# Kernel tuning notes

Measured on AMD Instinct MI355X. Metric: run time of the kernel, lower is better.

The kernel has to match this reference:

```python
import jax, jax.numpy as jnp
import numpy as np

B, C, H, W = 16, 128, 128, 128
NUM_HEADS, HEAD_DIM = 4, 32
HIDDEN = NUM_HEADS * HEAD_DIM  # 128
GROUPS = 32
EPS = 1e-5


def setup_inputs() -> dict:
    key = jax.random.key(0)
    ks = jax.random.split(key, 6)
    # conv1x1 weights: torch Conv2d weight (out, in, 1, 1) -> stored as (out, in)
    fan_qkv = C
    fan_proj = HIDDEN
    return {
        "x": jax.random.normal(ks[0], (B, C, H, W), dtype=jnp.float32),
        "gn_w": jnp.ones((C,), dtype=jnp.float32),
        "gn_b": jnp.zeros((C,), dtype=jnp.float32),
        "qkv_w": jax.random.normal(ks[1], (3 * HIDDEN, C), dtype=jnp.float32) / np.sqrt(fan_qkv),
        "proj_w": jax.random.normal(ks[2], (C, HIDDEN), dtype=jnp.float32) / np.sqrt(fan_proj),
        "proj_b": jax.random.normal(ks[3], (C,), dtype=jnp.float32) * 0.01,
    }


def reference(x, gn_w, gn_b, qkv_w, proj_w, proj_b):
    b, c, h, w = x.shape
    n = h * w
    residual = x
    # GroupNorm(32 groups), biased variance, affine
    xg = x.reshape(b, GROUPS, c // GROUPS, h, w)
    mu = xg.mean(axis=(2, 3, 4), keepdims=True)
    var = xg.var(axis=(2, 3, 4), keepdims=True)
    xn = ((xg - mu) * jax.lax.rsqrt(var + EPS)).reshape(b, c, h, w)
    xn = xn * gn_w[None, :, None, None] + gn_b[None, :, None, None]
    # 1x1 conv QKV (no bias); channel layout -> (b, 3, heads, head_dim, n)
    qkv = jnp.einsum('oc,bchw->bohw', qkv_w, xn)
    qkv = qkv.reshape(b, 3, NUM_HEADS, HEAD_DIM, n)
    q, k, v = qkv[:, 0], qkv[:, 1], qkv[:, 2]
    q = jax.nn.softmax(q, axis=-1)   # over spatial positions
    k = jax.nn.softmax(k, axis=-2)   # over head_dim
    # context = k @ v^T : (b,h,D,D)
    ctx = jnp.einsum('bhdn,bhen->bhde', k, v)
    # out = context^T @ q : (b,h,D,n)
    out = jnp.einsum('bhde,bhdn->bhen', ctx, q)
    out = out.reshape(b, HIDDEN, h, w)
    # 1x1 conv projection (with bias)
    out = jnp.einsum('co,bohw->bchw', proj_w, out) + proj_b[None, :, None, None]
    return out + residual
```

## Files before the change

### kernel.cpp

```cpp
#include <hip/hip_runtime.h>


#define B_ 16
#define C_ 128
#define N_ 16384

typedef short bf16x8 __attribute__((ext_vector_type(8)));
typedef float f32x4 __attribute__((ext_vector_type(4)));
typedef unsigned u32x2 __attribute__((ext_vector_type(2)));

__device__ __forceinline__ ushort f2bf(float f) {
    union { float f; unsigned u; } v; v.f = f;
    unsigned r = (v.u + 0x7FFFu + ((v.u >> 16) & 1u)) >> 16;
    return (ushort)r;
}
__device__ __forceinline__ float bf2f(unsigned h) {
    union { unsigned u; float f; } v; v.u = h << 16;
    return v.f;
}

__global__ void k_stats(const float* __restrict__ x, const float* __restrict__ gnw,
                        const float* __restrict__ gnb, float* __restrict__ sc,
                        float* __restrict__ bi,
                        const float* __restrict__ qkvw, ushort* __restrict__ wbf) {
    int bg = blockIdx.x;
    if (bg >= 512) {
        int i = (bg - 512) * 1024 + threadIdx.x;
        if (i < 384 * 128) wbf[i] = f2bf(qkvw[i]);
        return;
    }
    const float4* p = (const float4*)(x + (size_t)bg * (4 * N_));
    float s = 0.f, s2 = 0.f;
    for (int i = threadIdx.x; i < N_; i += 1024) {
        float4 v = p[i];
        s  += v.x + v.y + v.z + v.w;
        s2 += v.x * v.x + v.y * v.y + v.z * v.z + v.w * v.w;
    }
    #pragma unroll
    for (int d = 32; d > 0; d >>= 1) { s += __shfl_xor(s, d); s2 += __shfl_xor(s2, d); }
    __shared__ float ls[16], ls2[16];
    int wid = threadIdx.x >> 6, lane = threadIdx.x & 63;
    if (lane == 0) { ls[wid] = s; ls2[wid] = s2; }
    __syncthreads();
    if (threadIdx.x == 0) {
        float S = 0.f, S2 = 0.f;
        #pragma unroll
        for (int i = 0; i < 16; ++i) { S += ls[i]; S2 += ls2[i]; }
        float m = S / 65536.f;
        float var = S2 / 65536.f - m * m;
        float rs = rsqrtf(var + 1e-5f);
        int b = bg >> 5, g = bg & 31;
        #pragma unroll
        for (int i = 0; i < 4; ++i) {
            int c = g * 4 + i;
            float scv = rs * gnw[c];
            sc[b * 128 + c] = scv;
            bi[b * 128 + c] = gnb[c] - m * scv;
        }
    }
}


#define MFMA16(A, Bv, Cc) __builtin_amdgcn_mfma_f32_16x16x32_bf16(A, Bv, Cc, 0, 0, 0)

#define DO_Q(J, OT) do { \
    f32x4 acc = {0.f, 0.f, 0.f, 0.f}; \
    acc = MFMA16(wf[J][0], xb[0], acc); acc = MFMA16(wf[J][1], xb[1], acc); \
    acc = MFMA16(wf[J][2], xb[2], acc); acc = MFMA16(wf[J][3], xb[3], acc); \
    float e0 = __expf(acc[0]), e1 = __expf(acc[1]); \
    float e2 = __expf(acc[2]), e3 = __expf(acc[3]); \
    qacc[J][0] += e0; qacc[J][1] += e1; qacc[J][2] += e2; qacc[J][3] += e3; \
    u32x2 pkq; \
    pkq.x = (unsigned)f2bf(e0) | ((unsigned)f2bf(e1) << 16); \
    pkq.y = (unsigned)f2bf(e2) | ((unsigned)f2bf(e3) << 16); \
    *(u32x2*)(eqp + (OT) * 16) = pkq; \
} while (0)

#define DO_K(JLO, H) do { \
    f32x4 aL = {0.f, 0.f, 0.f, 0.f}, aH = {0.f, 0.f, 0.f, 0.f}; \
    aL = MFMA16(wf[JLO][0], xb[0], aL);     aH = MFMA16(wf[(JLO)+1][0], xb[0], aH); \
    aL = MFMA16(wf[JLO][1], xb[1], aL);     aH = MFMA16(wf[(JLO)+1][1], xb[1], aH); \
    aL = MFMA16(wf[JLO][2], xb[2], aL);     aH = MFMA16(wf[(JLO)+1][2], xb[2], aH); \
    aL = MFMA16(wf[JLO][3], xb[3], aL);     aH = MFMA16(wf[(JLO)+1][3], xb[3], aH); \
    float eL0 = __expf(aL[0]), eL1 = __expf(aL[1]), eL2 = __expf(aL[2]), eL3 = __expf(aL[3]); \
    float eH0 = __expf(aH[0]), eH1 = __expf(aH[1]), eH2 = __expf(aH[2]), eH3 = __expf(aH[3]); \
    float s = eL0 + eL1 + eL2 + eL3 + eH0 + eH1 + eH2 + eH3; \
    s += __shfl_xor(s, 16); s += __shfl_xor(s, 32); \
    float rinv = 1.f / s; \
    ksm[H][lg * 4 + 0][nloc] = f2bf(eL0 * rinv); \
    ksm[H][lg * 4 + 1][nloc] = f2bf(eL1 * rinv); \
    ksm[H][lg * 4 + 2][nloc] = f2bf(eL2 * rinv); \
    ksm[H][lg * 4 + 3][nloc] = f2bf(eL3 * rinv); \
    ksm[H][16 + lg * 4 + 0][nloc] = f2bf(eH0 * rinv); \
    ksm[H][16 + lg * 4 + 1][nloc] = f2bf(eH1 * rinv); \
    ksm[H][16 + lg * 4 + 2][nloc] = f2bf(eH2 * rinv); \
    ksm[H][16 + lg * 4 + 3][nloc] = f2bf(eH3 * rinv); \
} while (0)

#define DO_V(J, HV, EB) do { \
    f32x4 acc = {0.f, 0.f, 0.f, 0.f}; \
    acc = MFMA16(wf[J][0], xb[0], acc); acc = MFMA16(wf[J][1], xb[1], acc); \
    acc = MFMA16(wf[J][2], xb[2], acc); acc = MFMA16(wf[J][3], xb[3], acc); \
    vls[HV][(EB) + lg * 4 + 0][nloc] = f2bf(acc[0]); \
    vls[HV][(EB) + lg * 4 + 1][nloc] = f2bf(acc[1]); \
    vls[HV][(EB) + lg * 4 + 2][nloc] = f2bf(acc[2]); \
    vls[HV][(EB) + lg * 4 + 3][nloc] = f2bf(acc[3]); \
} while (0)

__global__ __launch_bounds__(256, 2) void k_main(
    const float* __restrict__ x, const ushort* __restrict__ wbf,
    const float* __restrict__ scA, const float* __restrict__ biA,
    ushort* __restrict__ eqT, float* __restrict__ qsumP, float* __restrict__ ctxP) {
    int blk = blockIdx.x;
    int b = blk >> 6, nb = blk & 63;
    int tid = threadIdx.x, wid = tid >> 6, lane = tid & 63;
    int l15 = lane & 15, lg = lane >> 4;

    __shared__ __align__(16) ushort xs[4096];
    __shared__ __align__(16) ushort ksm[4][32][40];
    __shared__ __align__(16) ushort vls[4][32][40];

    bf16x8 wf[6][4];
    {
        const ushort* wr = wbf + (size_t)(wid * 96 + l15) * 128 + lg * 8;
        #pragma unroll
        for (int j = 0; j < 6; ++j)
            #pragma unroll
            for (int kc = 0; kc < 4; ++kc)
                wf[j][kc] = *(const bf16x8*)(wr + j * 2048 + kc * 32);
    }

    float qacc[6][4];
    #pragma unroll
    for (int j = 0; j < 6; ++j)
        #pragma unroll
        for (int r = 0; r < 4; ++r) qacc[j][r] = 0.f;
    f32x4 cacc[2][2];
    #pragma unroll
    for (int di = 0; di < 2; ++di)
        #pragma unroll
        for (int ei = 0; ei < 2; ++ei) cacc[di][ei] = (f32x4){0.f, 0.f, 0.f, 0.f};

    const int pk_ = tid & 7, pcb = tid >> 3;
    const float* xrow = x + (size_t)b * (C_ * N_) + nb * 256 + pk_ * 4;
    float scv[4], biv[4];
    #pragma unroll
    for (int i = 0; i < 4; ++i) {
        scv[i] = scA[b * 128 + pcb * 4 + i];
        biv[i] = biA[b * 128 + pcb * 4 + i];
    }
    unsigned boffj[4];
    #pragma unroll
    for (int j = 0; j < 4; ++j) {
        int n = pk_ * 4 + j;
        boffj[j] = (unsigned)(n * 256 + (((pcb >> 1) * 16) ^ ((n & 7) << 4)) + (pcb & 1) * 8);
    }

    for (int ch = 0; ch < 8; ++ch) {
        __syncthreads();
        unsigned e[4][4];
        #pragma unroll
        for (int i = 0; i < 4; ++i) {
            float4 v = *(const float4*)(xrow + (size_t)(pcb * 4 + i) * N_ + ch * 32);
            float s = scv[i], t = biv[i];
            e[i][0] = f2bf(v.x * s + t);
            e[i][1] = f2bf(v.y * s + t);
            e[i][2] = f2bf(v.z * s + t);
            e[i][3] = f2bf(v.w * s + t);
        }
        #pragma unroll
        for (int j = 0; j < 4; ++j) {
            u32x2 wj;
            wj.x = e[0][j] | (e[1][j] << 16);
            wj.y = e[2][j] | (e[3][j] << 16);
            *(u32x2*)((char*)xs + boffj[j]) = wj;
        }
        __syncthreads();

        #pragma unroll
        for (int nt = 0; nt < 2; ++nt) {
            int row = nt * 16 + l15;
            bf16x8 xb[4];
            #pragma unroll
            for (int kc = 0; kc < 4; ++kc) {
                unsigned off = (unsigned)(row * 256 +
                    (((kc * 4 + lg) * 16) ^ ((row & 7) << 4)));
                xb[kc] = *(const bf16x8*)((const char*)xs + off);
            }
            int nloc = nt * 16 + l15;
            int ng = nb * 256 + ch * 32 + nloc;
            ushort* eqp = eqT + ((size_t)b * N_ + ng) * 128 + lg * 4;

            if (wid == 0) {
                DO_Q(0, 0); DO_Q(1, 1); DO_Q(2, 2); DO_Q(3, 3); DO_Q(4, 4); DO_Q(5, 5);
            } else if (wid == 1) {
                DO_Q(0, 6); DO_Q(1, 7); DO_K(2, 0); DO_K(4, 1);
            } else if (wid == 2) {
                DO_K(0, 2); DO_K(2, 3); DO_V(4, 0, 0); DO_V(5, 0, 16);
            } else {
                DO_V(0, 1, 0); DO_V(1, 1, 16); DO_V(2, 2, 0);
                DO_V(3, 2, 16); DO_V(4, 3, 0); DO_V(5, 3, 16);
            }
        }
        __syncthreads();

        {
            bf16x8 A0 = *(const bf16x8*)&ksm[wid][l15][lg * 8];
            bf16x8 A1 = *(const bf16x8*)&ksm[wid][16 + l15][lg * 8];
            bf16x8 B0 = *(const bf16x8*)&vls[wid][l15][lg * 8];
            bf16x8 B1 = *(const bf16x8*)&vls[wid][16 + l15][lg * 8];
            cacc[0][0] = MFMA16(A0, B0, cacc[0][0]);
            cacc[0][1] = MFMA16(A0, B1, cacc[0][1]);
            cacc[1][0] = MFMA16(A1, B0, cacc[1][0]);
            cacc[1][1] = MFMA16(A1, B1, cacc[1][1]);
        }
    }

    int nq = (wid == 0) ? 6 : (wid == 1 ? 2 : 0);
    #pragma unroll
    for (int j = 0; j < 6; ++j) {
        if (j < nq) {
            #pragma unroll
            for (int r = 0; r < 4; ++r) {
                float s = qacc[j][r];
                s += __shfl_xor(s, 1); s += __shfl_xor(s, 2);
                s += __shfl_xor(s, 4); s += __shfl_xor(s, 8);
                if (l15 == 0)
                    qsumP[(size_t)blk * 128 + (wid * 6 + j) * 16 + lg * 4 + r] = s;
            }
        }
    }
    float* cp = ctxP + (size_t)blk * 4096 + wid * 1024;
    #pragma unroll
    for (int di = 0; di < 2; ++di)
        #pragma unroll
        for (int ei = 0; ei < 2; ++ei)
            #pragma unroll
            for (int r = 0; r < 4; ++r)
                cp[(di * 16 + lg * 4 + r) * 32 + ei * 16 + l15] = cacc[di][ei][r];
}

__global__ void k_red(float* __restrict__ ctxP) {
    int blk = blockIdx.x;
    int b = blk >> 3, sl = blk & 7;
    float* base = ctxP + (size_t)b * 64 * 4096;
    #pragma unroll
    for (int r = 0; r < 2; ++r) {
        int i = sl * 512 + r * 256 + threadIdx.x;
        float s = 0.f;
        for (int q = 0; q < 64; ++q) s += base[(size_t)q * 4096 + i];
        base[i] = s;
    }
}

__global__ void k_comb(const float* __restrict__ ctxP, const float* __restrict__ qsumP,
                       const float* __restrict__ projw, ushort* __restrict__ mpp) {
    int b = blockIdx.x, tid = threadIdx.x;
    __shared__ float ctx[4096];
    __shared__ float qinv[128];
    for (int i = tid; i < 4096; i += 256)
        ctx[i] = ctxP[(size_t)b * 64 * 4096 + i];
    if (tid < 128) {
        float s = 0.f;
        const float* p = qsumP + (size_t)b * 64 * 128 + tid;
        for (int q = 0; q < 64; ++q) s += p[q * 128];
        qinv[tid] = 1.f / s;
    }
    __syncthreads();
    int c = tid >> 1, hd0 = (tid & 1) * 64;
    unsigned ow[32];
    for (int k = 0; k < 64; ++k) {
        int hd = hd0 + k, h = hd >> 5, d = hd & 31;
        const float* pw = projw + c * 128 + h * 32;
        const float* cx = ctx + h * 1024 + d * 32;
        float s = 0.f;
        #pragma unroll 8
        for (int e = 0; e < 32; ++e) s += pw[e] * cx[e];
        s *= qinv[hd];
        ushort bv = f2bf(s);
        if (k & 1) ow[k >> 1] |= ((unsigned)bv) << 16; else ow[k >> 1] = bv;
    }
    ushort* dst = mpp + ((size_t)(b * 128 + c)) * 128 + hd0;
    #pragma unroll
    for (int q = 0; q < 8; ++q) {
        uint4 t; t.x = ow[q * 4]; t.y = ow[q * 4 + 1]; t.z = ow[q * 4 + 2]; t.w = ow[q * 4 + 3];
        ((uint4*)dst)[q] = t;
    }
}

__global__ __launch_bounds__(256) void k_final(
    const ushort* __restrict__ eqT, const ushort* __restrict__ mpp,
    const float* __restrict__ projb, const float* __restrict__ x,
    float* __restrict__ out) {
    int blk = blockIdx.x;
    int b = blk >> 7, nb = blk & 127;
    int tid = threadIdx.x, wid = tid >> 6, lane = tid & 63;
    int l15 = lane & 15, lg = lane >> 4;

    __shared__ __align__(16) ushort att[16384];

    bf16x8 bm[2][4];
    #pragma unroll
    for (int ctk = 0; ctk < 2; ++ctk) {
        const ushort* br = mpp + ((size_t)(b * 128 + (wid * 2 + ctk) * 16 + l15)) * 128 + lg * 8;
        #pragma unroll
        for (int kc = 0; kc < 4; ++kc) bm[ctk][kc] = *(const bf16x8*)(br + kc * 32);
    }

    int n0 = nb * 128;
    #pragma unroll
    for (int nt = 0; nt < 8; ++nt) {
        const ushort* ar = eqT + ((size_t)b * N_ + n0 + nt * 16 + l15) * 128 + lg * 8;
        bf16x8 af[4];
        #pragma unroll
        for (int kc = 0; kc < 4; ++kc) af[kc] = *(const bf16x8*)(ar + kc * 32);
        #pragma unroll
        for (int ctk = 0; ctk < 2; ++ctk) {
            f32x4 a = {0.f, 0.f, 0.f, 0.f};
            #pragma unroll
            for (int kc = 0; kc < 4; ++kc) a = MFMA16(af[kc], bm[ctk][kc], a);
            int c = (wid * 2 + ctk) * 16 + l15;
            int nloc = nt * 16 + lg * 4;
            unsigned byte = (unsigned)(c * 256 + ((nloc * 2) ^ ((c & 15) << 4)));
            u32x2 pk;
            pk.x = (unsigned)f2bf(a[0]) | ((unsigned)f2bf(a[1]) << 16);
            pk.y = (unsigned)f2bf(a[2]) | ((unsigned)f2bf(a[3]) << 16);
            *(u32x2*)((char*)att + byte) = pk;
        }
    }
    __syncthreads();

    int crow = lane >> 5;
    int n4 = (lane & 31) * 4;
    #pragma unroll
    for (int it = 0; it < 16; ++it) {
        int c = wid * 32 + it * 2 + crow;
        unsigned byte = (unsigned)(c * 256 + ((n4 * 2) ^ ((c & 15) << 4)));
        u32x2 pk = *(const u32x2*)((const char*)att + byte);
        size_t off = (size_t)(b * C_ + c) * N_ + n0 + n4;
        f32x4 xv = __builtin_nontemporal_load((const f32x4*)(x + off));
        float pbv = projb[c];
        f32x4 o4;
        o4[0] = bf2f(pk.x & 0xffffu) + pbv + xv[0];
        o4[1] = bf2f(pk.x >> 16)     + pbv + xv[1];
        o4[2] = bf2f(pk.y & 0xffffu) + pbv + xv[2];
        o4[3] = bf2f(pk.y >> 16)     + pbv + xv[3];
        *(f32x4*)(out + off) = o4;
    }
}

extern "C" void kernel_launch(void* const* d_in, const int* in_sizes, int n_in,
                              void* d_out, int out_size, void* d_ws, size_t ws_size,
                              hipStream_t stream) {
    const float* x     = (const float*)d_in[0];
    const float* gnw   = (const float*)d_in[1];
    const float* gnb   = (const float*)d_in[2];
    const float* qkvw  = (const float*)d_in[3];
    const float* projw = (const float*)d_in[4];
    const float* projb = (const float*)d_in[5];
    float* out = (float*)d_out;

    char* ws = (char*)d_ws;
    ushort* wbf   = (ushort*)(ws);
    float*  qsumP = (float*)(ws + 102400);
    ushort* mpp   = (ushort*)(ws + 626688);
    float*  sc    = (float*)(ws + 626688);
    float*  bi    = (float*)(ws + 634880);
    float*  ctxP  = (float*)(ws + 1150976);
    ushort* eqT   = (ushort*)(ws + 17928192);

    k_stats<<<560,  1024, 0, stream>>>(x, gnw, gnb, sc, bi, qkvw, wbf);
    k_main <<<1024, 256,  0, stream>>>(x, wbf, sc, bi, eqT, qsumP, ctxP);
    k_red  <<<128,  256,  0, stream>>>(ctxP);
    k_comb <<<16,   256,  0, stream>>>(ctxP, qsumP, projw, mpp);
    k_final<<<2048, 256,  0, stream>>>(eqT, mpp, projb, x, out);
}
```

Measured before the change: 234.8 us.

## Recompute softmax-Q numerators in final kernel instead of storing eqT

k_main no longer writes the exp(q) tensor to global memory and only accumulates its column sums. k_final reloads x, applies the GroupNorm scale/bias, recomputes the Q projection and exponent into LDS, then applies the combined context/projection matrix. This removes a large bf16 intermediate's write and read traffic, at the cost of an extra x read and duplicated Q MFMA/exp work in k_final. The workspace is relaid out so scale/bias no longer alias the mpp buffer.

```diff
diff --git a/kernel.cpp b/kernel.cpp
--- a/kernel.cpp
+++ b/kernel.cpp
@@ -63,17 +63,12 @@
 
 #define MFMA16(A, Bv, Cc) __builtin_amdgcn_mfma_f32_16x16x32_bf16(A, Bv, Cc, 0, 0, 0)
 
-#define DO_Q(J, OT) do { \
+#define DO_Q(J) do { \
     f32x4 acc = {0.f, 0.f, 0.f, 0.f}; \
     acc = MFMA16(wf[J][0], xb[0], acc); acc = MFMA16(wf[J][1], xb[1], acc); \
     acc = MFMA16(wf[J][2], xb[2], acc); acc = MFMA16(wf[J][3], xb[3], acc); \
-    float e0 = __expf(acc[0]), e1 = __expf(acc[1]); \
-    float e2 = __expf(acc[2]), e3 = __expf(acc[3]); \
-    qacc[J][0] += e0; qacc[J][1] += e1; qacc[J][2] += e2; qacc[J][3] += e3; \
-    u32x2 pkq; \
-    pkq.x = (unsigned)f2bf(e0) | ((unsigned)f2bf(e1) << 16); \
-    pkq.y = (unsigned)f2bf(e2) | ((unsigned)f2bf(e3) << 16); \
-    *(u32x2*)(eqp + (OT) * 16) = pkq; \
+    qacc[J][0] += __expf(acc[0]); qacc[J][1] += __expf(acc[1]); \
+    qacc[J][2] += __expf(acc[2]); qacc[J][3] += __expf(acc[3]); \
 } while (0)
 
 #define DO_K(JLO, H) do { \
@@ -110,7 +105,7 @@
 __global__ __launch_bounds__(256, 2) void k_main(
     const float* __restrict__ x, const ushort* __restrict__ wbf,
     const float* __restrict__ scA, const float* __restrict__ biA,
-    ushort* __restrict__ eqT, float* __restrict__ qsumP, float* __restrict__ ctxP) {
+    float* __restrict__ qsumP, float* __restrict__ ctxP) {
     int blk = blockIdx.x;
     int b = blk >> 6, nb = blk & 63;
     int tid = threadIdx.x, wid = tid >> 6, lane = tid & 63;
@@ -188,13 +183,11 @@
                 xb[kc] = *(const bf16x8*)((const char*)xs + off);
             }
             int nloc = nt * 16 + l15;
-            int ng = nb * 256 + ch * 32 + nloc;
-            ushort* eqp = eqT + ((size_t)b * N_ + ng) * 128 + lg * 4;
 
             if (wid == 0) {
-                DO_Q(0, 0); DO_Q(1, 1); DO_Q(2, 2); DO_Q(3, 3); DO_Q(4, 4); DO_Q(5, 5);
+                DO_Q(0); DO_Q(1); DO_Q(2); DO_Q(3); DO_Q(4); DO_Q(5);
             } else if (wid == 1) {
-                DO_Q(0, 6); DO_Q(1, 7); DO_K(2, 0); DO_K(4, 1);
+                DO_Q(0); DO_Q(1); DO_K(2, 0); DO_K(4, 1);
             } else if (wid == 2) {
                 DO_K(0, 2); DO_K(2, 3); DO_V(4, 0, 0); DO_V(5, 0, 16);
             } else {
@@ -289,16 +282,28 @@
 }
 
 __global__ __launch_bounds__(256) void k_final(
-    const ushort* __restrict__ eqT, const ushort* __restrict__ mpp,
+    const ushort* __restrict__ wbf, const ushort* __restrict__ mpp,
+    const float* __restrict__ scA, const float* __restrict__ biA,
     const float* __restrict__ projb, const float* __restrict__ x,
     float* __restrict__ out) {
     int blk = blockIdx.x;
-    int b = blk >> 7, nb = blk & 127;
+    int b = blk >> 8, nb = blk & 255;
     int tid = threadIdx.x, wid = tid >> 6, lane = tid & 63;
     int l15 = lane & 15, lg = lane >> 4;
-
-    __shared__ __align__(16) ushort att[16384];
-
+    int n0 = nb * 64;
+
+    __shared__ __align__(16) char lds[32768];
+    ushort* xs   = (ushort*)lds;
+    ushort* att  = (ushort*)lds;
+    ushort* eqls = (ushort*)(lds + 16384);
+
+    bf16x8 wq[2][4];
+    #pragma unroll
+    for (int j = 0; j < 2; ++j) {
+        const ushort* wr = wbf + (size_t)((wid * 2 + j) * 16 + l15) * 128 + lg * 8;
+        #pragma unroll
+        for (int kc = 0; kc < 4; ++kc) wq[j][kc] = *(const bf16x8*)(wr + kc * 32);
+    }
     bf16x8 bm[2][4];
     #pragma unroll
     for (int ctk = 0; ctk < 2; ++ctk) {
@@ -307,35 +312,90 @@
         for (int kc = 0; kc < 4; ++kc) bm[ctk][kc] = *(const bf16x8*)(br + kc * 32);
     }
 
-    int n0 = nb * 128;
-    #pragma unroll
-    for (int nt = 0; nt < 8; ++nt) {
-        const ushort* ar = eqT + ((size_t)b * N_ + n0 + nt * 16 + l15) * 128 + lg * 8;
+    {
+        const int pk_ = tid & 15, pcb = tid >> 4;
+        const float* xrow = x + (size_t)b * (C_ * N_) + n0 + pk_ * 4;
+        unsigned e[8][4];
+        #pragma unroll
+        for (int i = 0; i < 8; ++i) {
+            int c = pcb * 8 + i;
+            float s = scA[b * 128 + c], t = biA[b * 128 + c];
+            float4 v = *(const float4*)(xrow + (size_t)c * N_);
+            e[i][0] = f2bf(v.x * s + t);
+            e[i][1] = f2bf(v.y * s + t);
+            e[i][2] = f2bf(v.z * s + t);
+            e[i][3] = f2bf(v.w * s + t);
+        }
+        #pragma unroll
+        for (int j = 0; j < 4; ++j) {
+            int n = pk_ * 4 + j;
+            uint4 wj;
+            wj.x = e[0][j] | (e[1][j] << 16);
+            wj.y = e[2][j] | (e[3][j] << 16);
+            wj.z = e[4][j] | (e[5][j] << 16);
+            wj.w = e[6][j] | (e[7][j] << 16);
+            unsigned byte = (unsigned)(n * 256 + ((pcb * 16) ^ ((n & 7) << 4)));
+            *(uint4*)((char*)xs + byte) = wj;
+        }
+    }
+    __syncthreads();
+
+    #pragma unroll
+    for (int nt = 0; nt < 4; ++nt) {
+        int row = nt * 16 + l15;
+        bf16x8 xb[4];
+        #pragma unroll
+        for (int kc = 0; kc < 4; ++kc) {
+            unsigned off = (unsigned)(row * 256 + (((kc * 4 + lg) * 16) ^ ((row & 7) << 4)));
+            xb[kc] = *(const bf16x8*)((const char*)xs + off);
+        }
+        #pragma unroll
+        for (int j = 0; j < 2; ++j) {
+            f32x4 a = {0.f, 0.f, 0.f, 0.f};
+            #pragma unroll
+            for (int kc = 0; kc < 4; ++kc) a = MFMA16(wq[j][kc], xb[kc], a);
+            u32x2 pk;
+            pk.x = (unsigned)f2bf(__expf(a[0])) | ((unsigned)f2bf(__expf(a[1])) << 16);
+            pk.y = (unsigned)f2bf(__expf(a[2])) | ((unsigned)f2bf(__expf(a[3])) << 16);
+            int ot = wid * 2 + j;
+            unsigned byte = (unsigned)(row * 256 +
+                (((ot * 2 + (lg >> 1)) * 16) ^ ((row & 7) << 4)) + (lg & 1) * 8);
+            *(u32x2*)((char*)eqls + byte) = pk;
+        }
+    }
+    __syncthreads();
+
+    #pragma unroll
+    for (int nt = 0; nt < 4; ++nt) {
+        int row = nt * 16 + l15;
         bf16x8 af[4];
         #pragma unroll
-        for (int kc = 0; kc < 4; ++kc) af[kc] = *(const bf16x8*)(ar + kc * 32);
+        for (int kc = 0; kc < 4; ++kc) {
+            unsigned off = (unsigned)(row * 256 + (((kc * 4 + lg) * 16) ^ ((row & 7) << 4)));
+            af[kc] = *(const bf16x8*)((const char*)eqls + off);
+        }
         #pragma unroll
         for (int ctk = 0; ctk < 2; ++ctk) {
             f32x4 a = {0.f, 0.f, 0.f, 0.f};
             #pragma unroll
             for (int kc = 0; kc < 4; ++kc) a = MFMA16(af[kc], bm[ctk][kc], a);
             int c = (wid * 2 + ctk) * 16 + l15;
-            int nloc = nt * 16 + lg * 4;
-            unsigned byte = (unsigned)(c * 256 + ((nloc * 2) ^ ((c & 15) << 4)));
             u32x2 pk;
             pk.x = (unsigned)f2bf(a[0]) | ((unsigned)f2bf(a[1]) << 16);
             pk.y = (unsigned)f2bf(a[2]) | ((unsigned)f2bf(a[3]) << 16);
+            unsigned byte = (unsigned)(c * 128 +
+                (((nt * 2 + (lg >> 1)) * 16) ^ ((c & 7) << 4)) + (lg & 1) * 8);
             *(u32x2*)((char*)att + byte) = pk;
         }
     }
     __syncthreads();
 
-    int crow = lane >> 5;
-    int n4 = (lane & 31) * 4;
-    #pragma unroll
-    for (int it = 0; it < 16; ++it) {
-        int c = wid * 32 + it * 2 + crow;
-        unsigned byte = (unsigned)(c * 256 + ((n4 * 2) ^ ((c & 15) << 4)));
+    int crow = lane >> 4;
+    int n4 = (lane & 15) * 4;
+    #pragma unroll
+    for (int it = 0; it < 8; ++it) {
+        int c = wid * 32 + it * 4 + crow;
+        unsigned byte = (unsigned)(c * 128 + ((n4 * 2) ^ ((c & 7) << 4)));
         u32x2 pk = *(const u32x2*)((const char*)att + byte);
         size_t off = (size_t)(b * C_ + c) * N_ + n0 + n4;
         f32x4 xv = __builtin_nontemporal_load((const f32x4*)(x + off));
@@ -364,14 +424,13 @@
     ushort* wbf   = (ushort*)(ws);
     float*  qsumP = (float*)(ws + 102400);
     ushort* mpp   = (ushort*)(ws + 626688);
-    float*  sc    = (float*)(ws + 626688);
-    float*  bi    = (float*)(ws + 634880);
-    float*  ctxP  = (float*)(ws + 1150976);
-    ushort* eqT   = (ushort*)(ws + 17928192);
+    float*  sc    = (float*)(ws + 1150976);
+    float*  bi    = (float*)(ws + 1159168);
+    float*  ctxP  = (float*)(ws + 1167360);
 
     k_stats<<<560,  1024, 0, stream>>>(x, gnw, gnb, sc, bi, qkvw, wbf);
-    k_main <<<1024, 256,  0, stream>>>(x, wbf, sc, bi, eqT, qsumP, ctxP);
+    k_main <<<1024, 256,  0, stream>>>(x, wbf, sc, bi, qsumP, ctxP);
     k_red  <<<128,  256,  0, stream>>>(ctxP);
     k_comb <<<16,   256,  0, stream>>>(ctxP, qsumP, projw, mpp);
-    k_final<<<2048, 256,  0, stream>>>(eqT, mpp, projb, x, out);
-}
+    k_final<<<4096, 256,  0, stream>>>(wbf, mpp, sc, bi, projb, x, out);
+}
```

Measured after the change: 215.4 us. -8.3%, faster.
